# Kernel optimization log

Measured on AMD Instinct MI355X. Metric: run time of the kernel, lower is better.

Reference implementation:

```python
import jax, jax.numpy as jnp
import numpy as np

B, T, C, H = 2, 2048, 1024, 16
HS = C // H  # head_size = 64
EPS = 1e-5


def setup_inputs() -> dict:
    key = jax.random.key(0)
    ks = jax.random.split(key, 12)
    s = 0.02
    return {
        "x": jax.random.normal(ks[0], (B, T, C), jnp.float32),
        # per-head q/k/v linears stacked on a leading head axis [H, C, HS]
        "Wq": jax.random.normal(ks[1], (H, C, HS), jnp.float32) * s,
        "bq": jnp.zeros((H, HS), jnp.float32),
        "Wk": jax.random.normal(ks[2], (H, C, HS), jnp.float32) * s,
        "bk": jnp.zeros((H, HS), jnp.float32),
        "Wv": jax.random.normal(ks[3], (H, C, HS), jnp.float32) * s,
        "bv": jnp.zeros((H, HS), jnp.float32),
        # output projection [H*HS, C] == [C, C]
        "Wo": jax.random.normal(ks[4], (C, C), jnp.float32) * s,
        "bo": jnp.zeros((C,), jnp.float32),
        # feed-forward: C -> 4C -> C
        "W1": jax.random.normal(ks[5], (C, 4 * C), jnp.float32) * s,
        "b1": jnp.zeros((4 * C,), jnp.float32),
        "W2": jax.random.normal(ks[6], (4 * C, C), jnp.float32) * s,
        "b2": jnp.zeros((C,), jnp.float32),
        # custom LayerNorm params (broadcast over last dim)
        "gamma1": jnp.ones((C,), jnp.float32),
        "beta1": jnp.zeros((C,), jnp.float32),
        "gamma2": jnp.ones((C,), jnp.float32),
        "beta2": jnp.zeros((C,), jnp.float32),
    }


def _ln(x, gamma, beta):
    # NOTE: faithful to the source: normalizes over axis=1 (the SEQUENCE axis
    # for [B,T,C] input), uses unbiased variance (torch default), and puts eps
    # OUTSIDE the sqrt: (x - mean) / (sqrt(var) + eps).
    mean = x.mean(axis=1, keepdims=True)
    var = x.var(axis=1, keepdims=True, ddof=1)
    return gamma * ((x - mean) / (jnp.sqrt(var) + EPS)) + beta


def reference(x, Wq, bq, Wk, bk, Wv, bv, Wo, bo, W1, b1, W2, b2,
              gamma1, beta1, gamma2, beta2):
    # --- self-attention sublayer (pre-norm, residual) ---
    h = _ln(x, gamma1, beta1)
    q = jnp.einsum('btc,hcd->bhtd', h, Wq) + bq[None, :, None, :]
    k = jnp.einsum('btc,hcd->bhtd', h, Wk) + bk[None, :, None, :]
    v = jnp.einsum('btc,hcd->bhtd', h, Wv) + bv[None, :, None, :]
    wei = jax.nn.softmax(jnp.einsum('bhtd,bhsd->bhts', q, k) * (HS ** -0.5), axis=-1)
    attn = jnp.einsum('bhts,bhsd->bhtd', wei, v)          # [B,H,T,HS]
    attn = attn.transpose(0, 2, 1, 3).reshape(B, T, H * HS)  # head-order concat
    x = x + attn @ Wo + bo
    # --- feed-forward sublayer (pre-norm, residual) ---
    h2 = _ln(x, gamma2, beta2)
    x = x + jax.nn.relu(h2 @ W1 + b1) @ W2 + b2
    return x
```

## Files before the change

kernel.cpp:

```cpp
#include <hip/hip_runtime.h>
#include <hip/hip_bf16.h>

#define Bq 2
#define Tq 2048
#define Cq 1024
#define Hq 16
#define HSq 64
#define EPSq 1e-5f

using bf16 = __hip_bfloat16;
using f32x4 = __attribute__((ext_vector_type(4))) float;
using f32x16 = __attribute__((ext_vector_type(16))) float;
using bf16x8 = __attribute__((ext_vector_type(8))) __bf16;

__device__ __forceinline__ bf16 f2bf(float f) { return __float2bfloat16(f); }
__device__ __forceinline__ unsigned short f2u(float f) {
    return __builtin_bit_cast(unsigned short, __float2bfloat16(f));
}
__device__ __forceinline__ void gload16(const void* g, void* l) {
    __builtin_amdgcn_global_load_lds((const __attribute__((address_space(1))) void*)g,
                                     (__attribute__((address_space(3))) void*)l, 16, 0, 0);
}

__global__ void k_transpose(const float* __restrict__ src, bf16* __restrict__ dst,
                            int R, int Cc, long strideSrc, long strideDst) {
    __shared__ bf16 tile[32][33];
    const long zb = blockIdx.z;
    src += zb * strideSrc;
    dst += zb * strideDst;
    int c0 = blockIdx.x * 32, r0 = blockIdx.y * 32;
    int tx = threadIdx.x & 31, ty = threadIdx.x >> 5;
    for (int i = ty; i < 32; i += 8)
        tile[i][tx] = f2bf(src[(long)(r0 + i) * Cc + (c0 + tx)]);
    __syncthreads();
    for (int i = ty; i < 32; i += 8)
        dst[(long)(c0 + i) * R + (r0 + tx)] = tile[tx][i];
}

__global__ void k_pack_bias(const float* __restrict__ a, const float* __restrict__ b,
                            const float* __restrict__ c, float* __restrict__ dst) {
    int i = blockIdx.x * 256 + threadIdx.x;
    dst[i] = a[i];
    dst[1024 + i] = b[i];
    dst[2048 + i] = c[i];
}

__global__ void k_ln_part(const float* __restrict__ x, float* __restrict__ ps,
                          float* __restrict__ pss) {
    int c = blockIdx.x * 256 + threadIdx.x;
    int b = blockIdx.y;
    int tc = blockIdx.z;
    const float* p = x + (long)b * Tq * Cq + (long)tc * 64 * Cq + c;
    float s = 0.f, ss = 0.f;
    for (int t = 0; t < 64; ++t) {
        float v = p[(long)t * Cq];
        s += v;
        ss += v * v;
    }
    long o = ((long)tc * Bq + b) * Cq + c;
    ps[o] = s;
    pss[o] = ss;
}

__global__ void k_ln_fin(const float* __restrict__ ps, const float* __restrict__ pss,
                         float* __restrict__ mean, float* __restrict__ rstd) {
    int i = blockIdx.x * 256 + threadIdx.x;
    float s = 0.f, ss = 0.f;
    for (int tc = 0; tc < 32; ++tc) {
        s += ps[(long)tc * (Bq * Cq) + i];
        ss += pss[(long)tc * (Bq * Cq) + i];
    }
    float m = s / (float)Tq;
    float var = (ss - s * m) / (float)(Tq - 1);
    var = fmaxf(var, 0.f);
    mean[i] = m;
    rstd[i] = 1.0f / (sqrtf(var) + EPSq);
}

__global__ void k_ln_apply(const float* __restrict__ x, const float* __restrict__ mean,
                           const float* __restrict__ rstd, const float* __restrict__ gamma,
                           const float* __restrict__ beta, bf16* __restrict__ out) {
    long i = (long)blockIdx.x * 256 + threadIdx.x;
    int c = (int)(i & (Cq - 1));
    long bt = i >> 10;
    int b = (int)(bt >> 11);
    float m = mean[b * Cq + c], r = rstd[b * Cq + c];
    out[i] = f2bf(gamma[c] * ((x[i] - m) * r) + beta[c]);
}

template <int MODE>
__global__ __launch_bounds__(256, 3) void k_gemm_nt(
    const bf16* __restrict__ A, int lda, const bf16* __restrict__ Bt, int ldb, int K,
    const float* __restrict__ bias, bf16* __restrict__ outB, int ldout) {
    __shared__ __bf16 sA[2][128 * 32];
    __shared__ __bf16 sB[2][128 * 32];
    const int m0 = blockIdx.y * 128, n0 = blockIdx.x * 128;
    const int tid = threadIdx.x;
    const int lane = tid & 63, wave = tid >> 6;
    const int lane15 = lane & 15, quad = lane >> 4;
    const int wm = (wave >> 1) * 64, wn = (wave & 1) * 64;
    const int srow = wave * 16 + (lane >> 2);
    const int scol = (lane & 3) * 8;
    __bf16* a00 = &sA[0][wave * 512];
    __bf16* a01 = &sA[0][2048 + wave * 512];
    __bf16* a10 = &sA[1][wave * 512];
    __bf16* a11 = &sA[1][2048 + wave * 512];
    __bf16* b00 = &sB[0][wave * 512];
    __bf16* b01 = &sB[0][2048 + wave * 512];
    __bf16* b10 = &sB[1][wave * 512];
    __bf16* b11 = &sB[1][2048 + wave * 512];
    const bf16* Ap = A + (long)(m0 + srow) * lda + scol;
    const bf16* Ap2 = Ap + 64L * lda;
    const bf16* Bp = Bt + (long)(n0 + srow) * ldb + scol;
    const bf16* Bp2 = Bp + 64L * ldb;

    f32x4 acc[4][4];
#pragma unroll
    for (int i = 0; i < 4; ++i)
#pragma unroll
        for (int j = 0; j < 4; ++j)
#pragma unroll
            for (int p = 0; p < 4; ++p) acc[i][j][p] = 0.f;

    for (int k0 = 0; k0 < K; k0 += 64) {
        __syncthreads();
        gload16(Ap + k0, a00);
        gload16(Ap2 + k0, a01);
        gload16(Ap + k0 + 32, a10);
        gload16(Ap2 + k0 + 32, a11);
        gload16(Bp + k0, b00);
        gload16(Bp2 + k0, b01);
        gload16(Bp + k0 + 32, b10);
        gload16(Bp2 + k0 + 32, b11);
        __syncthreads();
#pragma unroll
        for (int kk = 0; kk < 2; ++kk) {
            bf16x8 af[4], bfr[4];
#pragma unroll
            for (int i = 0; i < 4; ++i)
                af[i] = *(const bf16x8*)(&sA[kk][(wm + i * 16 + lane15) * 32 + quad * 8]);
#pragma unroll
            for (int j = 0; j < 4; ++j)
                bfr[j] = *(const bf16x8*)(&sB[kk][(wn + j * 16 + lane15) * 32 + quad * 8]);
#pragma unroll
            for (int i = 0; i < 4; ++i)
#pragma unroll
                for (int j = 0; j < 4; ++j)
                    acc[i][j] = __builtin_amdgcn_mfma_f32_16x16x32_bf16(af[i], bfr[j],
                                                                        acc[i][j], 0, 0, 0);
        }
    }
    if (MODE == 0) {
#pragma unroll
        for (int i = 0; i < 4; ++i) {
            const int mm = m0 + wm + i * 16 + quad * 4;
            const int b = mm >> 11, t4 = mm & (Tq - 1);
#pragma unroll
            for (int j = 0; j < 4; ++j) {
                const int n = n0 + wn + j * 16 + lane15;
                const int which = n >> 10, hh = (n >> 6) & (Hq - 1), d = n & (HSq - 1);
                const long bh = (long)b * Hq + hh;
                const float bb = bias[n];
                if (which == 0) {
#pragma unroll
                    for (int p = 0; p < 4; ++p)
                        outB[bh * 131072 + (long)(t4 + p) * HSq + d] =
                            f2bf((acc[i][j][p] + bb) * 0.125f);
                } else if (which == 1) {
#pragma unroll
                    for (int p = 0; p < 4; ++p)
                        outB[4194304L + bh * 131072 + (long)(t4 + p) * HSq + d] =
                            f2bf(acc[i][j][p] + bb);
                } else {
                    ushort4 pk;
                    pk.x = f2u(acc[i][j][0] + bb);
                    pk.y = f2u(acc[i][j][1] + bb);
                    pk.z = f2u(acc[i][j][2] + bb);
                    pk.w = f2u(acc[i][j][3] + bb);
                    *(ushort4*)(&outB[8388608L + bh * 131072 + (long)d * Tq + t4]) = pk;
                }
            }
        }
    } else {
#pragma unroll
        for (int i = 0; i < 4; ++i) {
#pragma unroll
            for (int p = 0; p < 4; ++p) {
                const int m = m0 + wm + i * 16 + quad * 4 + p;
#pragma unroll
                for (int j = 0; j < 4; ++j) {
                    const int n = n0 + wn + j * 16 + lane15;
                    outB[(long)m * ldout + n] = f2bf(fmaxf(acc[i][j][p] + bias[n], 0.f));
                }
            }
        }
    }
}

template <int MODE>
__global__ __launch_bounds__(256, 4) void k_gemm_n64(
    const bf16* __restrict__ A, int lda, const bf16* __restrict__ Bt, int ldb, int K,
    const float* __restrict__ bias, const float* __restrict__ residF,
    float* __restrict__ outF, int ldout) {
    __shared__ __bf16 sA[2][128 * 32];
    __shared__ __bf16 sB[2][64 * 32];
    const int m0 = blockIdx.y * 128, n0 = blockIdx.x * 64;
    const int tid = threadIdx.x;
    const int lane = tid & 63, wave = tid >> 6;
    const int lane15 = lane & 15, quad = lane >> 4;
    const int wm = wave * 32;
    const int srow = wave * 16 + (lane >> 2);
    const int scol = (lane & 3) * 8;
    __bf16* a00 = &sA[0][wave * 512];
    __bf16* a01 = &sA[0][2048 + wave * 512];
    __bf16* a10 = &sA[1][wave * 512];
    __bf16* a11 = &sA[1][2048 + wave * 512];
    __bf16* b00 = &sB[0][wave * 512];
    __bf16* b10 = &sB[1][wave * 512];
    const bf16* Ap = A + (long)(m0 + srow) * lda + scol;
    const bf16* Ap2 = Ap + 64L * lda;
    const bf16* Bp = Bt + (long)(n0 + srow) * ldb + scol;

    f32x4 acc[2][4];
#pragma unroll
    for (int i = 0; i < 2; ++i)
#pragma unroll
        for (int j = 0; j < 4; ++j)
#pragma unroll
            for (int p = 0; p < 4; ++p) acc[i][j][p] = 0.f;

    for (int k0 = 0; k0 < K; k0 += 64) {
        __syncthreads();
        gload16(Ap + k0, a00);
        gload16(Ap2 + k0, a01);
        gload16(Ap + k0 + 32, a10);
        gload16(Ap2 + k0 + 32, a11);
        gload16(Bp + k0, b00);
        gload16(Bp + k0 + 32, b10);
        __syncthreads();
#pragma unroll
        for (int kk = 0; kk < 2; ++kk) {
            bf16x8 af[2], bfr[4];
#pragma unroll
            for (int i = 0; i < 2; ++i)
                af[i] = *(const bf16x8*)(&sA[kk][(wm + i * 16 + lane15) * 32 + quad * 8]);
#pragma unroll
            for (int j = 0; j < 4; ++j)
                bfr[j] = *(const bf16x8*)(&sB[kk][(j * 16 + lane15) * 32 + quad * 8]);
#pragma unroll
            for (int i = 0; i < 2; ++i)
#pragma unroll
                for (int j = 0; j < 4; ++j)
                    acc[i][j] = __builtin_amdgcn_mfma_f32_16x16x32_bf16(af[i], bfr[j],
                                                                        acc[i][j], 0, 0, 0);
        }
    }
#pragma unroll
    for (int i = 0; i < 2; ++i) {
#pragma unroll
        for (int p = 0; p < 4; ++p) {
            const int m = m0 + wm + i * 16 + quad * 4 + p;
#pragma unroll
            for (int j = 0; j < 4; ++j) {
                const int n = n0 + j * 16 + lane15;
                outF[(long)m * ldout + n] =
                    acc[i][j][p] + bias[n] + residF[(long)m * ldout + n];
            }
        }
    }
}

__global__ __launch_bounds__(256, 2) void k_attn(const bf16* __restrict__ qkv,
                                                 bf16* __restrict__ attn) {
    __shared__ __bf16 sK[64 * 72];
    __shared__ __bf16 sVt[64 * 72];
    const int bh = blockIdx.y;
    const int q0 = blockIdx.x * 128;
    const int tid = threadIdx.x, wave = tid >> 6, lane = tid & 63;
    const int lane31 = lane & 31, laneh = lane >> 5;
    const bf16* Qp = qkv + (long)bh * 131072;
    const bf16* Kp = qkv + 4194304L + (long)bh * 131072;
    const bf16* Vtp = qkv + 8388608L + (long)bh * 131072;
    bf16x8 qa[4];
#pragma unroll
    for (int s = 0; s < 4; ++s)
        qa[s] = *(const bf16x8*)(&Qp[(long)(q0 + wave * 32 + lane31) * HSq + s * 16 + laneh * 8]);
    f32x16 o[2];
#pragma unroll
    for (int dt = 0; dt < 2; ++dt)
#pragma unroll
        for (int r = 0; r < 16; ++r) o[dt][r] = 0.f;
    float rs = 0.f;
    const int r0 = tid >> 3, c0 = (tid & 7) * 8;
    const int r1 = r0 + 32;

    uint4 nk0 = *(const uint4*)(&Kp[(long)r0 * HSq + c0]);
    uint4 nk1 = *(const uint4*)(&Kp[(long)r1 * HSq + c0]);
    uint4 nv0 = *(const uint4*)(&Vtp[(long)r0 * Tq + c0]);
    uint4 nv1 = *(const uint4*)(&Vtp[(long)r1 * Tq + c0]);

    for (int kc = 0; kc < Tq; kc += 64) {
        __syncthreads();
        *(uint4*)(&sK[r0 * 72 + c0]) = nk0;
        *(uint4*)(&sK[r1 * 72 + c0]) = nk1;
        *(uint4*)(&sVt[r0 * 72 + c0]) = nv0;
        *(uint4*)(&sVt[r1 * 72 + c0]) = nv1;
        __syncthreads();
        if (kc + 64 < Tq) {
            nk0 = *(const uint4*)(&Kp[(long)(kc + 64 + r0) * HSq + c0]);
            nk1 = *(const uint4*)(&Kp[(long)(kc + 64 + r1) * HSq + c0]);
            nv0 = *(const uint4*)(&Vtp[(long)r0 * Tq + kc + 64 + c0]);
            nv1 = *(const uint4*)(&Vtp[(long)r1 * Tq + kc + 64 + c0]);
        }
#pragma unroll
        for (int nt = 0; nt < 2; ++nt) {
            f32x16 z;
#pragma unroll
            for (int r = 0; r < 16; ++r) z[r] = 0.f;
#pragma unroll
            for (int s = 0; s < 4; ++s) {
                bf16x8 kb =
                    *(const bf16x8*)(&sK[(nt * 32 + lane31) * 72 + s * 16 + laneh * 8]);
                z = __builtin_amdgcn_mfma_f32_32x32x16_bf16(kb, qa[s], z, 0, 0, 0);
            }
            float e[16];
#pragma unroll
            for (int r = 0; r < 16; ++r) {
                e[r] = __expf(z[r]);
                rs += e[r];
            }
            unsigned int pk[8];
#pragma unroll
            for (int g = 0; g < 4; ++g)
#pragma unroll
                for (int h = 0; h < 2; ++h)
                    pk[g * 2 + h] = (unsigned int)f2u(e[g * 4 + 2 * h]) |
                                    ((unsigned int)f2u(e[g * 4 + 2 * h + 1]) << 16);
            unsigned int sa0 = laneh ? pk[0] : pk[2], sa1 = laneh ? pk[1] : pk[3];
            unsigned int ra0 = __shfl_xor((int)sa0, 32), ra1 = __shfl_xor((int)sa1, 32);
            unsigned int sb0 = laneh ? pk[4] : pk[6], sb1 = laneh ? pk[5] : pk[7];
            unsigned int rb0 = __shfl_xor((int)sb0, 32), rb1 = __shfl_xor((int)sb1, 32);
            uint4 f0, f1;
            if (laneh == 0) {
                f0 = {pk[0], pk[1], ra0, ra1};
                f1 = {pk[4], pk[5], rb0, rb1};
            } else {
                f0 = {ra0, ra1, pk[2], pk[3]};
                f1 = {rb0, rb1, pk[6], pk[7]};
            }
            bf16x8 pa0 = __builtin_bit_cast(bf16x8, f0);
            bf16x8 pa1 = __builtin_bit_cast(bf16x8, f1);
#pragma unroll
            for (int dt = 0; dt < 2; ++dt) {
                bf16x8 vb0 =
                    *(const bf16x8*)(&sVt[(dt * 32 + lane31) * 72 + nt * 32 + laneh * 8]);
                bf16x8 vb1 = *(const bf16x8*)(&sVt[(dt * 32 + lane31) * 72 + nt * 32 + 16 +
                                                   laneh * 8]);
                o[dt] = __builtin_amdgcn_mfma_f32_32x32x16_bf16(pa0, vb0, o[dt], 0, 0, 0);
                o[dt] = __builtin_amdgcn_mfma_f32_32x32x16_bf16(pa1, vb1, o[dt], 0, 0, 0);
            }
        }
    }
    float ltot = rs + __shfl_xor(rs, 32);
    float linv = 1.0f / ltot;
    const int b = bh >> 4, hh = bh & 15;
#pragma unroll
    for (int r = 0; r < 16; ++r) {
        const int tl = (r & 3) + 8 * (r >> 2) + 4 * laneh;
        float inv = __shfl(linv, tl);
        const int t = q0 + wave * 32 + tl;
        const long base = ((long)b * Tq + t) * Cq + hh * HSq;
#pragma unroll
        for (int dt = 0; dt < 2; ++dt)
            attn[base + dt * 32 + lane31] = f2bf(o[dt][r] * inv);
    }
}

extern "C" void kernel_launch(void* const* d_in, const int* in_sizes, int n_in,
                              void* d_out, int out_size, void* d_ws, size_t ws_size,
                              hipStream_t stream) {
    const float* x = (const float*)d_in[0];
    const float* Wq = (const float*)d_in[1];
    const float* bqv = (const float*)d_in[2];
    const float* Wk = (const float*)d_in[3];
    const float* bkv = (const float*)d_in[4];
    const float* Wv = (const float*)d_in[5];
    const float* bvv = (const float*)d_in[6];
    const float* Wo = (const float*)d_in[7];
    const float* bo = (const float*)d_in[8];
    const float* W1 = (const float*)d_in[9];
    const float* b1 = (const float*)d_in[10];
    const float* W2 = (const float*)d_in[11];
    const float* b2 = (const float*)d_in[12];
    const float* g1 = (const float*)d_in[13];
    const float* be1 = (const float*)d_in[14];
    const float* g2 = (const float*)d_in[15];
    const float* be2 = (const float*)d_in[16];

    char* ws = (char*)d_ws;
    size_t off = 0;
    auto alloc = [&](size_t bytes) {
        void* p = ws + off;
        off += (bytes + 255) & ~(size_t)255;
        return p;
    };
    bf16* regA = (bf16*)alloc(32L * 1024 * 1024);
    float* x2 = (float*)alloc(4096L * 1024 * 4);
    bf16* buf1 = (bf16*)alloc(4096L * 1024 * 2);
    float* bqkv = (float*)alloc(3072L * 4);
    float* ps = (float*)alloc(32L * Bq * Cq * 4);
    float* pss = (float*)alloc(32L * Bq * Cq * 4);
    float* mean1 = (float*)alloc(Bq * Cq * 4);
    float* rstd1 = (float*)alloc(Bq * Cq * 4);
    float* mean2 = (float*)alloc(Bq * Cq * 4);
    float* rstd2 = (float*)alloc(Bq * Cq * 4);
    bf16* dres = (bf16*)d_out;
    float* outF = (float*)d_out;

    k_ln_part<<<dim3(4, Bq, 32), 256, 0, stream>>>(x, ps, pss);
    k_ln_fin<<<dim3(8), 256, 0, stream>>>(ps, pss, mean1, rstd1);
    k_ln_apply<<<dim3(16384), 256, 0, stream>>>(x, mean1, rstd1, g1, be1, dres);

    k_transpose<<<dim3(2, 32, 16), 256, 0, stream>>>(Wq, buf1, 1024, 64, 65536, 65536);
    k_transpose<<<dim3(2, 32, 16), 256, 0, stream>>>(Wk, buf1 + 1048576, 1024, 64, 65536, 65536);
    k_transpose<<<dim3(2, 32, 16), 256, 0, stream>>>(Wv, buf1 + 2097152, 1024, 64, 65536, 65536);
    k_pack_bias<<<dim3(4), 256, 0, stream>>>(bqv, bkv, bvv, bqkv);
    k_gemm_nt<0><<<dim3(24, 32), 256, 0, stream>>>(dres, 1024, buf1, 1024, 1024, bqkv, regA, 0);
    k_attn<<<dim3(16, 32), 256, 0, stream>>>(regA, dres);
    k_transpose<<<dim3(32, 32, 1), 256, 0, stream>>>(Wo, buf1, 1024, 1024, 0, 0);
    k_gemm_n64<1><<<dim3(16, 32), 256, 0, stream>>>(dres, 1024, buf1, 1024, 1024, bo, x, x2,
                                                    1024);
    k_ln_part<<<dim3(4, Bq, 32), 256, 0, stream>>>(x2, ps, pss);
    k_ln_fin<<<dim3(8), 256, 0, stream>>>(ps, pss, mean2, rstd2);
    k_ln_apply<<<dim3(16384), 256, 0, stream>>>(x2, mean2, rstd2, g2, be2, dres);

    k_transpose<<<dim3(128, 32, 1), 256, 0, stream>>>(W1, buf1, 1024, 4096, 0, 0);
    k_gemm_nt<2><<<dim3(32, 32), 256, 0, stream>>>(dres, 1024, buf1, 1024, 1024, b1, regA, 4096);
    k_transpose<<<dim3(32, 128, 1), 256, 0, stream>>>(W2, buf1, 4096, 1024, 0, 0);
    k_gemm_n64<3><<<dim3(16, 32), 256, 0, stream>>>(regA, 4096, buf1, 4096, 4096, b2, x2, outF,
                                                    1024);
}
```

Measured before the change: 391.6 us.

## Double-buffer output GEMMs, swizzle LDS and XCD block order, prioritize attention MFMAs

Replaces the 128x64 n64 GEMM used for the Wo and W2 projections with a 128x128 tile kernel. That kernel prefetches the next K-slice into a second LDS buffer while computing on the current one, removing a barrier per iteration. It also XOR-swizzles the LDS column layout in both GEMM kernels to reduce bank conflicts, and remaps block IDs across XCDs to improve L2 locality. The attention kernel raises wave priority around its MFMA sections. The larger tiles double LDS use and halve the number of blocks (256 for the output GEMMs), which may reduce occupancy and load balance.

```diff
diff --git a/kernel.cpp b/kernel.cpp
--- a/kernel.cpp
+++ b/kernel.cpp
@@ -88,19 +88,31 @@
     out[i] = f2bf(gamma[c] * ((x[i] - m) * r) + beta[c]);
 }
 
+__device__ __forceinline__ void xcd_swizzle(int& bx, int& by) {
+    const int gx = gridDim.x;
+    const int nwg = gx * gridDim.y;
+    const int bid = blockIdx.y * gx + blockIdx.x;
+    const int swz = (bid & 7) * (nwg >> 3) + (bid >> 3);
+    bx = swz % gx;
+    by = swz / gx;
+}
+
 template <int MODE>
 __global__ __launch_bounds__(256, 3) void k_gemm_nt(
     const bf16* __restrict__ A, int lda, const bf16* __restrict__ Bt, int ldb, int K,
     const float* __restrict__ bias, bf16* __restrict__ outB, int ldout) {
     __shared__ __bf16 sA[2][128 * 32];
     __shared__ __bf16 sB[2][128 * 32];
-    const int m0 = blockIdx.y * 128, n0 = blockIdx.x * 128;
+    int bx, by;
+    xcd_swizzle(bx, by);
+    const int m0 = by * 128, n0 = bx * 128;
     const int tid = threadIdx.x;
     const int lane = tid & 63, wave = tid >> 6;
     const int lane15 = lane & 15, quad = lane >> 4;
     const int wm = (wave >> 1) * 64, wn = (wave & 1) * 64;
     const int srow = wave * 16 + (lane >> 2);
-    const int scol = (lane & 3) * 8;
+    const int scol = (((lane & 3) ^ ((lane >> 3) & 3)) * 8);
+    const int sq8 = (quad ^ ((lane15 >> 1) & 3)) * 8;
     __bf16* a00 = &sA[0][wave * 512];
     __bf16* a01 = &sA[0][2048 + wave * 512];
     __bf16* a10 = &sA[1][wave * 512];
@@ -138,10 +150,10 @@
             bf16x8 af[4], bfr[4];
 #pragma unroll
             for (int i = 0; i < 4; ++i)
-                af[i] = *(const bf16x8*)(&sA[kk][(wm + i * 16 + lane15) * 32 + quad * 8]);
+                af[i] = *(const bf16x8*)(&sA[kk][(wm + i * 16 + lane15) * 32 + sq8]);
 #pragma unroll
             for (int j = 0; j < 4; ++j)
-                bfr[j] = *(const bf16x8*)(&sB[kk][(wn + j * 16 + lane15) * 32 + quad * 8]);
+                bfr[j] = *(const bf16x8*)(&sB[kk][(wn + j * 16 + lane15) * 32 + sq8]);
 #pragma unroll
             for (int i = 0; i < 4; ++i)
 #pragma unroll
@@ -197,72 +209,83 @@
     }
 }
 
-template <int MODE>
-__global__ __launch_bounds__(256, 4) void k_gemm_n64(
+__global__ __launch_bounds__(256, 2) void k_gemm_pf(
     const bf16* __restrict__ A, int lda, const bf16* __restrict__ Bt, int ldb, int K,
     const float* __restrict__ bias, const float* __restrict__ residF,
     float* __restrict__ outF, int ldout) {
-    __shared__ __bf16 sA[2][128 * 32];
-    __shared__ __bf16 sB[2][64 * 32];
-    const int m0 = blockIdx.y * 128, n0 = blockIdx.x * 64;
+    __shared__ __bf16 sA[2][2][128 * 32];
+    __shared__ __bf16 sB[2][2][128 * 32];
+    int bx, by;
+    xcd_swizzle(bx, by);
+    const int m0 = by * 128, n0 = bx * 128;
     const int tid = threadIdx.x;
     const int lane = tid & 63, wave = tid >> 6;
     const int lane15 = lane & 15, quad = lane >> 4;
-    const int wm = wave * 32;
+    const int wm = (wave >> 1) * 64, wn = (wave & 1) * 64;
     const int srow = wave * 16 + (lane >> 2);
-    const int scol = (lane & 3) * 8;
-    __bf16* a00 = &sA[0][wave * 512];
-    __bf16* a01 = &sA[0][2048 + wave * 512];
-    __bf16* a10 = &sA[1][wave * 512];
-    __bf16* a11 = &sA[1][2048 + wave * 512];
-    __bf16* b00 = &sB[0][wave * 512];
-    __bf16* b10 = &sB[1][wave * 512];
+    const int scol = (((lane & 3) ^ ((lane >> 3) & 3)) * 8);
+    const int sq8 = (quad ^ ((lane15 >> 1) & 3)) * 8;
     const bf16* Ap = A + (long)(m0 + srow) * lda + scol;
     const bf16* Ap2 = Ap + 64L * lda;
     const bf16* Bp = Bt + (long)(n0 + srow) * ldb + scol;
-
-    f32x4 acc[2][4];
-#pragma unroll
-    for (int i = 0; i < 2; ++i)
+    const bf16* Bp2 = Bp + 64L * ldb;
+
+    f32x4 acc[4][4];
+#pragma unroll
+    for (int i = 0; i < 4; ++i)
 #pragma unroll
         for (int j = 0; j < 4; ++j)
 #pragma unroll
             for (int p = 0; p < 4; ++p) acc[i][j][p] = 0.f;
 
-    for (int k0 = 0; k0 < K; k0 += 64) {
+#define STAGE_PF(p, ko)                                      \
+    do {                                                     \
+        gload16(Ap + (ko), &sA[p][0][wave * 512]);           \
+        gload16(Ap2 + (ko), &sA[p][0][2048 + wave * 512]);   \
+        gload16(Ap + (ko) + 32, &sA[p][1][wave * 512]);      \
+        gload16(Ap2 + (ko) + 32, &sA[p][1][2048 + wave * 512]); \
+        gload16(Bp + (ko), &sB[p][0][wave * 512]);           \
+        gload16(Bp2 + (ko), &sB[p][0][2048 + wave * 512]);   \
+        gload16(Bp + (ko) + 32, &sB[p][1][wave * 512]);      \
+        gload16(Bp2 + (ko) + 32, &sB[p][1][2048 + wave * 512]); \
+    } while (0)
+
+#define COMPUTE_PF(p)                                                                   \
+    do {                                                                                \
+        _Pragma("unroll") for (int kk = 0; kk < 2; ++kk) {                              \
+            bf16x8 af[4], bfr[4];                                                       \
+            _Pragma("unroll") for (int i = 0; i < 4; ++i) af[i] =                       \
+                *(const bf16x8*)(&sA[p][kk][(wm + i * 16 + lane15) * 32 + sq8]);        \
+            _Pragma("unroll") for (int j = 0; j < 4; ++j) bfr[j] =                      \
+                *(const bf16x8*)(&sB[p][kk][(wn + j * 16 + lane15) * 32 + sq8]);        \
+            _Pragma("unroll") for (int i = 0; i < 4; ++i)                               \
+                _Pragma("unroll") for (int j = 0; j < 4; ++j) acc[i][j] =               \
+                    __builtin_amdgcn_mfma_f32_16x16x32_bf16(af[i], bfr[j], acc[i][j],   \
+                                                            0, 0, 0);                   \
+        }                                                                               \
+    } while (0)
+
+    STAGE_PF(0, 0);
+    __syncthreads();
+    int cur = 0;
+    for (int k0 = 0; k0 < K - 64; k0 += 64) {
+        STAGE_PF(cur ^ 1, k0 + 64);
+        COMPUTE_PF(cur);
         __syncthreads();
-        gload16(Ap + k0, a00);
-        gload16(Ap2 + k0, a01);
-        gload16(Ap + k0 + 32, a10);
-        gload16(Ap2 + k0 + 32, a11);
-        gload16(Bp + k0, b00);
-        gload16(Bp + k0 + 32, b10);
-        __syncthreads();
-#pragma unroll
-        for (int kk = 0; kk < 2; ++kk) {
-            bf16x8 af[2], bfr[4];
-#pragma unroll
-            for (int i = 0; i < 2; ++i)
-                af[i] = *(const bf16x8*)(&sA[kk][(wm + i * 16 + lane15) * 32 + quad * 8]);
-#pragma unroll
-            for (int j = 0; j < 4; ++j)
-                bfr[j] = *(const bf16x8*)(&sB[kk][(j * 16 + lane15) * 32 + quad * 8]);
-#pragma unroll
-            for (int i = 0; i < 2; ++i)
-#pragma unroll
-                for (int j = 0; j < 4; ++j)
-                    acc[i][j] = __builtin_amdgcn_mfma_f32_16x16x32_bf16(af[i], bfr[j],
-                                                                        acc[i][j], 0, 0, 0);
-        }
-    }
-#pragma unroll
-    for (int i = 0; i < 2; ++i) {
+        cur ^= 1;
+    }
+    COMPUTE_PF(cur);
+#undef STAGE_PF
+#undef COMPUTE_PF
+
+#pragma unroll
+    for (int i = 0; i < 4; ++i) {
 #pragma unroll
         for (int p = 0; p < 4; ++p) {
             const int m = m0 + wm + i * 16 + quad * 4 + p;
 #pragma unroll
             for (int j = 0; j < 4; ++j) {
-                const int n = n0 + j * 16 + lane15;
+                const int n = n0 + wn + j * 16 + lane15;
                 outF[(long)m * ldout + n] =
                     acc[i][j][p] + bias[n] + residF[(long)m * ldout + n];
             }
@@ -317,12 +340,14 @@
             f32x16 z;
 #pragma unroll
             for (int r = 0; r < 16; ++r) z[r] = 0.f;
+            __builtin_amdgcn_s_setprio(1);
 #pragma unroll
             for (int s = 0; s < 4; ++s) {
                 bf16x8 kb =
                     *(const bf16x8*)(&sK[(nt * 32 + lane31) * 72 + s * 16 + laneh * 8]);
                 z = __builtin_amdgcn_mfma_f32_32x32x16_bf16(kb, qa[s], z, 0, 0, 0);
             }
+            __builtin_amdgcn_s_setprio(0);
             float e[16];
 #pragma unroll
             for (int r = 0; r < 16; ++r) {
@@ -350,6 +375,7 @@
             }
             bf16x8 pa0 = __builtin_bit_cast(bf16x8, f0);
             bf16x8 pa1 = __builtin_bit_cast(bf16x8, f1);
+            __builtin_amdgcn_s_setprio(1);
 #pragma unroll
             for (int dt = 0; dt < 2; ++dt) {
                 bf16x8 vb0 =
@@ -359,6 +385,7 @@
                 o[dt] = __builtin_amdgcn_mfma_f32_32x32x16_bf16(pa0, vb0, o[dt], 0, 0, 0);
                 o[dt] = __builtin_amdgcn_mfma_f32_32x32x16_bf16(pa1, vb1, o[dt], 0, 0, 0);
             }
+            __builtin_amdgcn_s_setprio(0);
         }
     }
     float ltot = rs + __shfl_xor(rs, 32);
@@ -428,8 +455,7 @@
     k_gemm_nt<0><<<dim3(24, 32), 256, 0, stream>>>(dres, 1024, buf1, 1024, 1024, bqkv, regA, 0);
     k_attn<<<dim3(16, 32), 256, 0, stream>>>(regA, dres);
     k_transpose<<<dim3(32, 32, 1), 256, 0, stream>>>(Wo, buf1, 1024, 1024, 0, 0);
-    k_gemm_n64<1><<<dim3(16, 32), 256, 0, stream>>>(dres, 1024, buf1, 1024, 1024, bo, x, x2,
-                                                    1024);
+    k_gemm_pf<<<dim3(8, 32), 256, 0, stream>>>(dres, 1024, buf1, 1024, 1024, bo, x, x2, 1024);
     k_ln_part<<<dim3(4, Bq, 32), 256, 0, stream>>>(x2, ps, pss);
     k_ln_fin<<<dim3(8), 256, 0, stream>>>(ps, pss, mean2, rstd2);
     k_ln_apply<<<dim3(16384), 256, 0, stream>>>(x2, mean2, rstd2, g2, be2, dres);
@@ -437,6 +463,6 @@
     k_transpose<<<dim3(128, 32, 1), 256, 0, stream>>>(W1, buf1, 1024, 4096, 0, 0);
     k_gemm_nt<2><<<dim3(32, 32), 256, 0, stream>>>(dres, 1024, buf1, 1024, 1024, b1, regA, 4096);
     k_transpose<<<dim3(32, 128, 1), 256, 0, stream>>>(W2, buf1, 4096, 1024, 0, 0);
-    k_gemm_n64<3><<<dim3(16, 32), 256, 0, stream>>>(regA, 4096, buf1, 4096, 4096, b2, x2, outF,
-                                                    1024);
-}
+    k_gemm_pf<<<dim3(8, 32), 256, 0, stream>>>(regA, 4096, buf1, 4096, 4096, b2, x2, outF,
+                                               1024);
+}
```

New measurement: 416.8 us. 1.06x slower.
